# Optimization experiments

Measured on AMD Instinct MI355X. Metric: run time of the kernel, lower is better.

Reference implementation:

```python
import jax, jax.numpy as jnp
import numpy as np

B = 1024       # n_nodes
C = 128        # num_features (multiplicity of 0e in irreps_in)
L = 16         # num_ell = dim of coupling irreps 0e+1o+2e+3o
E = 10         # num_elements
Q = 3          # num_equivariance for 1o output (2*lmax+1)
# path counts (last dim of U tensors) per correlation order nu=1,2,3
P_0e = (1, 4, 23)
P_1o = (1, 6, 37)


def setup_inputs() -> dict:
    key = jax.random.key(0)
    ks = jax.random.split(key, 16)
    x = jax.random.normal(ks[0], (B, C, L), dtype=jnp.float32)
    elem = jax.random.randint(ks[1], (B,), 0, E)
    y = jax.nn.one_hot(elem, E, dtype=jnp.float32)  # one-hot element types
    # U tensors are constant (buffer) CG-derived coupling tensors; random stand-ins
    # with the exact shapes produced by U_matrix_real.
    U1_0e = jax.random.normal(ks[2], (L, P_0e[0]), dtype=jnp.float32)
    U2_0e = jax.random.normal(ks[3], (L, L, P_0e[1]), dtype=jnp.float32)
    U3_0e = jax.random.normal(ks[4], (L, L, L, P_0e[2]), dtype=jnp.float32)
    U1_1o = jax.random.normal(ks[5], (Q, L, P_1o[0]), dtype=jnp.float32)
    U2_1o = jax.random.normal(ks[6], (Q, L, L, P_1o[1]), dtype=jnp.float32)
    U3_1o = jax.random.normal(ks[7], (Q, L, L, L, P_1o[2]), dtype=jnp.float32)
    # per-element weights, init randn/num_params as in the torch module
    W1_0e = jax.random.normal(ks[8], (E, P_0e[0], C), dtype=jnp.float32) / P_0e[0]
    W2_0e = jax.random.normal(ks[9], (E, P_0e[1], C), dtype=jnp.float32) / P_0e[1]
    W3_0e = jax.random.normal(ks[10], (E, P_0e[2], C), dtype=jnp.float32) / P_0e[2]
    W1_1o = jax.random.normal(ks[11], (Q and E, P_1o[0], C), dtype=jnp.float32) / P_1o[0]
    W1_1o = jax.random.normal(ks[11], (E, P_1o[0], C), dtype=jnp.float32) / P_1o[0]
    W2_1o = jax.random.normal(ks[12], (E, P_1o[1], C), dtype=jnp.float32) / P_1o[1]
    W3_1o = jax.random.normal(ks[13], (E, P_1o[2], C), dtype=jnp.float32) / P_1o[2]
    return dict(x=x, y=y,
                U1_0e=U1_0e, U2_0e=U2_0e, U3_0e=U3_0e,
                W1_0e=W1_0e, W2_0e=W2_0e, W3_0e=W3_0e,
                U1_1o=U1_1o, U2_1o=U2_1o, U3_1o=U3_1o,
                W1_1o=W1_1o, W2_1o=W2_1o, W3_1o=W3_1o)


def _contract_0e(x, y, U1, U2, U3, W1, W2, W3):
    # correlation order 3 chain for a scalar (0e) output irrep
    out = jnp.einsum('wxik,ekc,bci,be->bcwx', U3, W3, x, y)            # [B,C,L,L]
    c = jnp.einsum('wxk,ekc,be->bcwx', U2, W2, y) + out
    out = jnp.einsum('bcwi,bci->bcw', c, x)                            # [B,C,L]
    c = jnp.einsum('wk,ekc,be->bcw', U1, W1, y) + out
    out = jnp.einsum('bci,bci->bc', c, x)                              # [B,C]
    return out


def _contract_1o(x, y, U1, U2, U3, W1, W2, W3):
    # correlation order 3 chain for a vector (1o) output irrep; w = equivariance dim (3)
    out = jnp.einsum('wxvik,ekc,bci,be->bcwxv', U3, W3, x, y)          # [B,C,3,L,L]
    c = jnp.einsum('wxvk,ekc,be->bcwxv', U2, W2, y) + out
    out = jnp.einsum('bcwxi,bci->bcwx', c, x)                          # [B,C,3,L]
    c = jnp.einsum('wxk,ekc,be->bcwx', U1, W1, y) + out
    out = jnp.einsum('bcwi,bci->bcw', c, x)                            # [B,C,3]
    return out.reshape(out.shape[0], -1)                                # [B,3C]


def reference(x, y, U1_0e, U2_0e, U3_0e, W1_0e, W2_0e, W3_0e,
              U1_1o, U2_1o, U3_1o, W1_1o, W2_1o, W3_1o):
    out0 = _contract_0e(x, y, U1_0e, U2_0e, U3_0e, W1_0e, W2_0e, W3_0e)
    out1 = _contract_1o(x, y, U1_1o, U2_1o, U3_1o, W1_1o, W2_1o, W3_1o)
    return jnp.concatenate([out0, out1], axis=-1)                       # [B, 4C]
```

## Files before the change

kernel.cpp:

```cpp
#include <hip/hip_runtime.h>

namespace {
constexpr int NB = 1024, NC = 128, NL = 16, NE = 10, NOUT = 4 * NC;
constexpr int NTHREADS = 256;
constexpr int NSPLIT = 2;
constexpr int P3_0 = 23, P2_0 = 4, P3_1 = 37, P2_1 = 6;
constexpr int TRI_P = 1040, DUO_P = 160, CSTRIDE = 1224;
constexpr int U3ROWS = P3_0 + 3 * P3_1;
constexpr int U2ROWS = P2_0 + 3 * P2_1;
constexpr int SYM3_FLOATS = U3ROWS * TRI_P;
constexpr int SYM2_FLOATS = U2ROWS * DUO_P;
constexpr int SYM_TOTAL = SYM3_FLOATS + SYM2_FLOATS;
constexpr int OFF_CNT = 0;
constexpr int OFF_NID = 16;
constexpr int OFF_SYM3A = 10272;
constexpr int OFF_SYM2A = OFF_SYM3A + SYM3_FLOATS;
constexpr int WS_REQ = OFF_SYM2A + SYM2_FLOATS;
}

__device__ __forceinline__ bool tri_from_padded(int t, int& ri, int& rj, int& rm) {
    int pos = 0;
    for (int i = 0; i < 16; ++i)
        for (int j = i; j < 16; ++j) {
            const int L = 16 - j, PL = (L + 3) & ~3;
            if (t < pos + PL) { ri = i; rj = j; rm = j + (t - pos); return (t - pos) < L; }
            pos += PL;
        }
    return false;
}
__device__ __forceinline__ bool duo_from_padded(int t, int& ri, int& rj) {
    int pos = 0;
    for (int i = 0; i < 16; ++i) {
        const int L = 16 - i, PL = (L + 3) & ~3;
        if (t < pos + PL) { ri = i; rj = i + (t - pos); return (t - pos) < L; }
        pos += PL;
    }
    return false;
}

__device__ __forceinline__ void sym_body(int n,
    const float* __restrict__ U3_0e, const float* __restrict__ U3_1o,
    const float* __restrict__ U2_0e, const float* __restrict__ U2_1o,
    float* __restrict__ dst) {
    if (n < SYM3_FLOATS) {
        const int kk = n / TRI_P, t = n - kk * TRI_P;
        int pass, k, P; const float* U;
        if (kk < P3_0) { pass = 0; k = kk; P = P3_0; U = U3_0e; }
        else { const int r = kk - P3_0; pass = 1 + r / P3_1; k = r - (pass - 1) * P3_1;
               P = P3_1; U = U3_1o + (size_t)(pass - 1) * 4096 * P3_1; }
        int i, j, m; float s = 0.f;
        if (tri_from_padded(t, i, j, m)) {
            auto u3 = [&](int a, int b, int c) {
                return U[(size_t)(((a << 4) + b) * 16 + c) * P + k]; };
            s = u3(i, j, m);
            if (i == j && j == m) {}
            else if (i == j) s += u3(i, m, i) + u3(m, i, i);
            else if (j == m) s += u3(j, i, j) + u3(j, j, i);
            else s += u3(i, m, j) + u3(j, i, m) + u3(j, m, i) + u3(m, i, j) + u3(m, j, i);
        }
        dst[n] = s;
    } else if (n < SYM_TOTAL) {
        const int r = n - SYM3_FLOATS;
        const int kk = r / DUO_P, t = r - kk * DUO_P;
        int pass, k, P; const float* U;
        if (kk < P2_0) { pass = 0; k = kk; P = P2_0; U = U2_0e; }
        else { const int q = kk - P2_0; pass = 1 + q / P2_1; k = q - (pass - 1) * P2_1;
               P = P2_1; U = U2_1o + (size_t)(pass - 1) * 256 * P2_1; }
        int i, j; float s = 0.f;
        if (duo_from_padded(t, i, j)) {
            auto u2 = [&](int a, int b) { return U[(size_t)((a << 4) + b) * P + k]; };
            s = u2(i, j) + (i < j ? u2(j, i) : 0.f);
        }
        dst[n] = s;
    }
}

__global__ void prep_kernel(const float* __restrict__ y,
                            const float* __restrict__ U3_0e, const float* __restrict__ U3_1o,
                            const float* __restrict__ U2_0e, const float* __restrict__ U2_1o,
                            float* __restrict__ ws) {
    const int bid = blockIdx.x, tid = threadIdx.x;
    if (bid < NE) {
        __shared__ int s_scan[NTHREADS];
        const int e = bid;
        unsigned pat = 0;
#pragma unroll
        for (int q = 0; q < 4; ++q)
            if (y[(tid * 4 + q) * NE + e] > 0.5f) pat |= (1u << q);
        const int lc = __popc(pat);
        s_scan[tid] = lc;
        __syncthreads();
#pragma unroll
        for (int off = 1; off < NTHREADS; off <<= 1) {
            const int add = (tid >= off) ? s_scan[tid - off] : 0;
            __syncthreads();
            s_scan[tid] += add;
            __syncthreads();
        }
        int* cnt = (int*)ws + OFF_CNT;
        int* nid = (int*)ws + OFF_NID + e * NB;
        int pos = s_scan[tid] - lc;
#pragma unroll
        for (int q = 0; q < 4; ++q)
            if (pat & (1u << q)) nid[pos++] = tid * 4 + q;
        if (tid == 0) cnt[e] = s_scan[NTHREADS - 1];
    } else {
        const int n = (bid - NE) * NTHREADS + tid;
        sym_body(n, U3_0e, U3_1o, U2_0e, U2_1o, ws + OFF_SYM3A);
    }
}

template <int P3c, int P2c>
__device__ __forceinline__ void build_lds(const float* __restrict__ sym3p,
                                          const float* __restrict__ sym2p,
                                          const float* __restrict__ s_w3,
                                          const float* __restrict__ s_w2,
                                          float* __restrict__ s_lds, int tid)
{
#pragma unroll 1
    for (int idx = tid; idx < (TRI_P / 4) * 2; idx += NTHREADS) {
        const int t4 = idx >> 1, cp = idx & 1;
        float aLx = 0, aLy = 0, aLz = 0, aLw = 0;
        float aHx = 0, aHy = 0, aHz = 0, aHw = 0;
#pragma unroll 4
        for (int k = 0; k < P3c; ++k) {
            const float4 u = *reinterpret_cast<const float4*>(sym3p + (size_t)k * TRI_P + 4 * t4);
            const float wL = s_w3[4 * k + 2 * cp];
            const float wH = s_w3[4 * k + 2 * cp + 1];
            aLx = fmaf(u.x, wL, aLx); aLy = fmaf(u.y, wL, aLy);
            aLz = fmaf(u.z, wL, aLz); aLw = fmaf(u.w, wL, aLw);
            aHx = fmaf(u.x, wH, aHx); aHy = fmaf(u.y, wH, aHy);
            aHz = fmaf(u.z, wH, aHz); aHw = fmaf(u.w, wH, aHw);
        }
        *reinterpret_cast<float4*>(s_lds + (2 * cp) * CSTRIDE + 4 * t4) =
            make_float4(aLx, aLy, aLz, aLw);
        *reinterpret_cast<float4*>(s_lds + (2 * cp + 1) * CSTRIDE + 4 * t4) =
            make_float4(aHx, aHy, aHz, aHw);
    }
    if (tid < (DUO_P / 4) * 2) {
        const int t4 = tid >> 1, cp = tid & 1;
        float aLx = 0, aLy = 0, aLz = 0, aLw = 0;
        float aHx = 0, aHy = 0, aHz = 0, aHw = 0;
#pragma unroll
        for (int k = 0; k < P2c; ++k) {
            const float4 u = *reinterpret_cast<const float4*>(sym2p + (size_t)k * DUO_P + 4 * t4);
            const float wL = s_w2[4 * k + 2 * cp];
            const float wH = s_w2[4 * k + 2 * cp + 1];
            aLx = fmaf(u.x, wL, aLx); aLy = fmaf(u.y, wL, aLy);
            aLz = fmaf(u.z, wL, aLz); aLw = fmaf(u.w, wL, aLw);
            aHx = fmaf(u.x, wH, aHx); aHy = fmaf(u.y, wH, aHy);
            aHz = fmaf(u.z, wH, aHz); aHw = fmaf(u.w, wH, aHw);
        }
        *reinterpret_cast<float4*>(s_lds + (2 * cp) * CSTRIDE + TRI_P + 4 * t4) =
            make_float4(aLx, aLy, aLz, aLw);
        *reinterpret_cast<float4*>(s_lds + (2 * cp + 1) * CSTRIDE + TRI_P + 4 * t4) =
            make_float4(aHx, aHy, aHz, aHw);
    }
}

__global__ void __launch_bounds__(NTHREADS, 4) node_kernel(
    const float* __restrict__ x, const float* __restrict__ ws,
    const float* __restrict__ U1_0e, const float* __restrict__ U1_1o,
    const float* __restrict__ W1_0e, const float* __restrict__ W2_0e,
    const float* __restrict__ W3_0e,
    const float* __restrict__ W1_1o, const float* __restrict__ W2_1o,
    const float* __restrict__ W3_1o,
    float* __restrict__ out) {
    __shared__ __align__(16) float s_lds[4 * CSTRIDE];
    __shared__ __align__(16) float s_w3[4 * P3_1];
    __shared__ __align__(16) float s_w2[4 * P2_1];
    __shared__ int s_nid[NB];
    const int tid = threadIdx.x, bid = blockIdx.x;
    const int pass = bid / (NE * (NC / 4));
    const int rest = bid % (NE * (NC / 4));
    const int e = rest / (NC / 4);
    const int cg = (rest % (NC / 4)) * 4;

    const int P3c = pass == 0 ? P3_0 : P3_1;
    const int P2c = pass == 0 ? P2_0 : P2_1;
    const int k3b = pass == 0 ? 0 : P3_0 + (pass - 1) * P3_1;
    const int k2b = pass == 0 ? 0 : P2_0 + (pass - 1) * P2_1;
    const float* W3e = (pass == 0 ? W3_0e + (size_t)e * P3_0 * NC
                                  : W3_1o + (size_t)e * P3_1 * NC) + cg;
    const float* W2e = (pass == 0 ? W2_0e + (size_t)e * P2_0 * NC
                                  : W2_1o + (size_t)e * P2_1 * NC) + cg;
    const float* W1e = (pass == 0 ? W1_0e : W1_1o) + e * NC + cg;
    const float* U1p = pass == 0 ? U1_0e : U1_1o + (pass - 1) * NL;
    const float* sym3p = ws + OFF_SYM3A + (size_t)k3b * TRI_P;
    const float* sym2p = ws + OFF_SYM2A + (size_t)k2b * DUO_P;

    const int* cnt = (const int*)ws + OFF_CNT;
    const int* nid = (const int*)ws + OFF_NID + e * NB;
    const int nn = cnt[e];
    for (int i = tid; i < nn; i += NTHREADS) s_nid[i] = nid[i];

    if (tid < P3c) {
        *reinterpret_cast<float4*>(&s_w3[4 * tid]) =
            *reinterpret_cast<const float4*>(W3e + tid * NC);
    } else if (tid >= 64 && tid < 64 + P2c) {
        const int k = tid - 64;
        *reinterpret_cast<float4*>(&s_w2[4 * k]) =
            *reinterpret_cast<const float4*>(W2e + k * NC);
    } else if (tid >= 128 && tid < 192) {
        const int t = tid - 128;
        s_lds[(t >> 4) * CSTRIDE + 1200 + (t & 15)] = U1p[t & 15] * W1e[t >> 4];
    }
    __syncthreads();

    if (pass == 0) build_lds<P3_0, P2_0>(sym3p, sym2p, s_w3, s_w2, s_lds, tid);
    else           build_lds<P3_1, P2_1>(sym3p, sym2p, s_w3, s_w2, s_lds, tid);
    __syncthreads();

    const int w = tid >> 6;
    const int lane = tid & 63;
    const int cc = cg + w;
    const float* Tch = s_lds + w * CSTRIDE;
    const int col = pass == 0 ? cc : NC + 3 * cc + (pass - 1);

#pragma unroll 1
    for (int base = 0; base < nn; base += 64) {
        const int slot = base + lane;
        const bool val = slot < nn;
        const int b = s_nid[val ? slot : 0];
        const float* xp = x + ((size_t)b * NC + cc) * NL;
        float xr[NL];
#pragma unroll
        for (int v4 = 0; v4 < 4; ++v4)
            reinterpret_cast<float4*>(xr)[v4] = reinterpret_cast<const float4*>(xp)[v4];

        float acc = 0.f;
        int t3 = 0, t2 = 0;
#pragma unroll
        for (int i = 0; i < 16; ++i) {
            float gi = Tch[1200 + i];
            const int L2 = 16 - i, PL2 = (L2 + 3) & ~3;
            float s2r[16];
#pragma unroll
            for (int q4 = 0; q4 < PL2 / 4; ++q4)
                reinterpret_cast<float4*>(s2r)[q4] =
                    *reinterpret_cast<const float4*>(Tch + TRI_P + t2 + 4 * q4);
            t2 += PL2;
#pragma unroll
            for (int jo = 0; jo < 16 - i; ++jo) {
                const int j = i + jo;
                float wv = s2r[jo];
                const int Lr = 16 - j, PLr = (Lr + 3) & ~3;
#pragma unroll
                for (int q4 = 0; q4 < PLr / 4; ++q4) {
                    const float4 tv = *reinterpret_cast<const float4*>(Tch + t3 + 4 * q4);
                    wv = fmaf(tv.x, xr[(j + 4 * q4 + 0) & 15], wv);
                    wv = fmaf(tv.y, xr[(j + 4 * q4 + 1) & 15], wv);
                    wv = fmaf(tv.z, xr[(j + 4 * q4 + 2) & 15], wv);
                    wv = fmaf(tv.w, xr[(j + 4 * q4 + 3) & 15], wv);
                }
                t3 += PLr;
                gi = fmaf(wv, xr[j], gi);
            }
            acc = fmaf(gi, xr[i], acc);
        }
        if (val) out[(size_t)b * NOUT + col] = acc;
    }
}

template <int P3, int P2>
__device__ __forceinline__ void build_gather_f(const float* __restrict__ U3,
                                               const float* __restrict__ U2,
                                               const float* __restrict__ s_w3,
                                               const float* __restrict__ s_w2,
                                               float* __restrict__ lds, int tid) {
#pragma unroll 1
    for (int t = tid; t < TRI_P; t += NTHREADS) {
        int i, j, m; const bool v = tri_from_padded(t, i, j, m);
        float a0 = 0, a1 = 0, a2 = 0, a3 = 0;
        if (v) {
            int ng = 1, g1 = 0, g2 = 0, g3 = 0, g4 = 0, g5 = 0;
            const int g0 = ((i * 16 + j) * 16 + m);
            if (i == j && j == m) { ng = 1; }
            else if (i == j) { g1 = ((i * 16 + m) * 16 + i); g2 = ((m * 16 + i) * 16 + i); ng = 3; }
            else if (j == m) { g1 = ((j * 16 + i) * 16 + j); g2 = ((j * 16 + j) * 16 + i); ng = 3; }
            else { g1 = ((i * 16 + m) * 16 + j); g2 = ((j * 16 + i) * 16 + m);
                   g3 = ((j * 16 + m) * 16 + i); g4 = ((m * 16 + i) * 16 + j);
                   g5 = ((m * 16 + j) * 16 + i); ng = 6; }
#pragma unroll 1
            for (int k = 0; k < P3; ++k) {
                float u = U3[(size_t)g0 * P3 + k];
                if (ng > 1) u += U3[(size_t)g1 * P3 + k] + U3[(size_t)g2 * P3 + k];
                if (ng == 6) u += U3[(size_t)g3 * P3 + k] + U3[(size_t)g4 * P3 + k]
                                + U3[(size_t)g5 * P3 + k];
                const float4 wk = reinterpret_cast<const float4*>(s_w3)[k];
                a0 = fmaf(u, wk.x, a0); a1 = fmaf(u, wk.y, a1);
                a2 = fmaf(u, wk.z, a2); a3 = fmaf(u, wk.w, a3);
            }
        }
        lds[0 * CSTRIDE + t] = a0; lds[1 * CSTRIDE + t] = a1;
        lds[2 * CSTRIDE + t] = a2; lds[3 * CSTRIDE + t] = a3;
    }
    if (tid < DUO_P) {
        int i, j; const bool v = duo_from_padded(tid, i, j);
        float a0 = 0, a1 = 0, a2 = 0, a3 = 0;
        if (v) {
#pragma unroll 1
            for (int k = 0; k < P2; ++k) {
                float u = U2[(size_t)((i << 4) + j) * P2 + k];
                if (i < j) u += U2[(size_t)((j << 4) + i) * P2 + k];
                const float4 wk = reinterpret_cast<const float4*>(s_w2)[k];
                a0 = fmaf(u, wk.x, a0); a1 = fmaf(u, wk.y, a1);
                a2 = fmaf(u, wk.z, a2); a3 = fmaf(u, wk.w, a3);
            }
        }
        lds[0 * CSTRIDE + TRI_P + tid] = a0; lds[1 * CSTRIDE + TRI_P + tid] = a1;
        lds[2 * CSTRIDE + TRI_P + tid] = a2; lds[3 * CSTRIDE + TRI_P + tid] = a3;
    }
}

__global__ void __launch_bounds__(NTHREADS, 4) symcon_fallback(
    const float* __restrict__ x, const float* __restrict__ y,
    const float* __restrict__ U1_0e, const float* __restrict__ U2_0e,
    const float* __restrict__ U3_0e,
    const float* __restrict__ W1_0e, const float* __restrict__ W2_0e,
    const float* __restrict__ W3_0e,
    const float* __restrict__ U1_1o, const float* __restrict__ U2_1o,
    const float* __restrict__ U3_1o,
    const float* __restrict__ W1_1o, const float* __restrict__ W2_1o,
    const float* __restrict__ W3_1o,
    float* __restrict__ out)
{
    __shared__ __align__(16) float s_lds[4 * CSTRIDE];
    __shared__ __align__(16) float s_w3[4 * P3_1 + 4];
    __shared__ __align__(16) float s_w2[4 * P2_1];
    __shared__ int s_nid[NB];
    __shared__ int s_scan[NTHREADS];

    const int tid = threadIdx.x;
    const int bid = blockIdx.x;
    const int s   = bid & 1;
    const int e   = (bid >> 1) % NE;
    const int cg  = (bid / (2 * NE)) * 4;

    unsigned pat = 0;
#pragma unroll
    for (int q = 0; q < 4; ++q)
        if (y[(tid * 4 + q) * NE + e] > 0.5f) pat |= (1u << q);
    const int lc = __popc(pat);
    s_scan[tid] = lc;
    __syncthreads();
#pragma unroll
    for (int off = 1; off < NTHREADS; off <<= 1) {
        const int add = (tid >= off) ? s_scan[tid - off] : 0;
        __syncthreads();
        s_scan[tid] += add;
        __syncthreads();
    }
    const int nn = s_scan[NTHREADS - 1];
    {
        int pos = s_scan[tid] - lc;
#pragma unroll
        for (int q = 0; q < 4; ++q)
            if (pat & (1u << q)) s_nid[pos++] = tid * 4 + q;
    }
    __syncthreads();

    const int half = (nn + 1) >> 1;
    const int l0 = s * half, l1 = min(nn, l0 + half);
    const int L = l1 - l0;
    if (L <= 0) return;

    const int w    = tid >> 6;
    const int ch   = (tid >> 4) & 3;
    const int nsub = tid & 15;
    const int cc   = cg + ch;
    const int chunk = (L + 3) >> 2;
    const int wbase = l0 + w * chunk;
    const int wend  = min(l1, wbase + chunk);
    const int iters = (chunk + 15) >> 4;
    const float* Tch = s_lds + ch * CSTRIDE;

#pragma unroll 1
    for (int pass = 0; pass < 4; ++pass) {
        const float* U3r = pass == 0 ? U3_0e : U3_1o + (size_t)(pass - 1) * 4096 * P3_1;
        const float* U2r = pass == 0 ? U2_0e : U2_1o + (size_t)(pass - 1) * 256 * P2_1;
        const float* U1p = (pass == 0 ? U1_0e : U1_1o + (pass - 1) * NL);
        const float* W3e = (pass == 0 ? W3_0e + (size_t)e * P3_0 * NC
                                      : W3_1o + (size_t)e * P3_1 * NC) + cg;
        const float* W2e = (pass == 0 ? W2_0e + (size_t)e * P2_0 * NC
                                      : W2_1o + (size_t)e * P2_1 * NC) + cg;
        const float* W1e = (pass == 0 ? W1_0e : W1_1o) + e * NC + cg;
        const int P3c = pass == 0 ? P3_0 : P3_1;
        const int P2c = pass == 0 ? P2_0 : P2_1;
        const int col = pass == 0 ? cc : NC + 3 * cc + (pass - 1);

        if (tid < 4 * P3c) {
            s_w3[tid] = W3e[(tid >> 2) * NC + (tid & 3)];
        } else if (tid >= 152 && tid < 152 + 4 * P2c) {
            const int t = tid - 152;
            s_w2[t] = W2e[(t >> 2) * NC + (t & 3)];
        } else if (tid >= 192) {
            const int t = tid - 192;
            s_lds[(t >> 4) * CSTRIDE + 1200 + (t & 15)] = U1p[t & 15] * W1e[t >> 4];
        }
        __syncthreads();

        if (pass == 0) build_gather_f<P3_0, P2_0>(U3r, U2r, s_w3, s_w2, s_lds, tid);
        else           build_gather_f<P3_1, P2_1>(U3r, U2r, s_w3, s_w2, s_lds, tid);
        __syncthreads();

#pragma unroll 1
        for (int it = 0; it < iters; ++it) {
            const int slot = wbase + it * 16 + nsub;
            const bool val = slot < wend;
            const int b = s_nid[val ? slot : l0];
            const float* xp = x + ((size_t)b * NC + cc) * NL;
            float xr[NL];
#pragma unroll
            for (int v4 = 0; v4 < 4; ++v4)
                reinterpret_cast<float4*>(xr)[v4] = reinterpret_cast<const float4*>(xp)[v4];

            float acc = 0.f;
            int t3 = 0, t2 = 0;
#pragma unroll
            for (int i = 0; i < 16; ++i) {
                float gi = Tch[1200 + i];
                const int L2 = 16 - i, PL2 = (L2 + 3) & ~3;
                float s2r[16];
#pragma unroll
                for (int q4 = 0; q4 < PL2 / 4; ++q4)
                    reinterpret_cast<float4*>(s2r)[q4] =
                        *reinterpret_cast<const float4*>(Tch + TRI_P + t2 + 4 * q4);
                t2 += PL2;
#pragma unroll
                for (int jo = 0; jo < 16 - i; ++jo) {
                    const int j = i + jo;
                    float wv = s2r[jo];
                    const int Lr = 16 - j, PLr = (Lr + 3) & ~3;
#pragma unroll
                    for (int q4 = 0; q4 < PLr / 4; ++q4) {
                        const float4 tv = *reinterpret_cast<const float4*>(Tch + t3 + 4 * q4);
                        wv = fmaf(tv.x, xr[(j + 4 * q4 + 0) & 15], wv);
                        wv = fmaf(tv.y, xr[(j + 4 * q4 + 1) & 15], wv);
                        wv = fmaf(tv.z, xr[(j + 4 * q4 + 2) & 15], wv);
                        wv = fmaf(tv.w, xr[(j + 4 * q4 + 3) & 15], wv);
                    }
                    t3 += PLr;
                    gi = fmaf(wv, xr[j], gi);
                }
                acc = fmaf(gi, xr[i], acc);
            }
            if (val) out[(size_t)b * NOUT + col] = acc;
        }
        __syncthreads();
    }
}

extern "C" void kernel_launch(void* const* d_in, const int* in_sizes, int n_in,
                              void* d_out, int out_size, void* d_ws, size_t ws_size,
                              hipStream_t stream) {
    const float* x     = (const float*)d_in[0];
    const float* y     = (const float*)d_in[1];
    const float* U1_0e = (const float*)d_in[2];
    const float* U2_0e = (const float*)d_in[3];
    const float* U3_0e = (const float*)d_in[4];
    const float* W1_0e = (const float*)d_in[5];
    const float* W2_0e = (const float*)d_in[6];
    const float* W3_0e = (const float*)d_in[7];
    const float* U1_1o = (const float*)d_in[8];
    const float* U2_1o = (const float*)d_in[9];
    const float* U3_1o = (const float*)d_in[10];
    const float* W1_1o = (const float*)d_in[11];
    const float* W2_1o = (const float*)d_in[12];
    const float* W3_1o = (const float*)d_in[13];
    float* out = (float*)d_out;
    float* ws = (float*)d_ws;

    if (ws_size >= (size_t)WS_REQ * sizeof(float)) {
        const int symBlocks = (SYM_TOTAL + NTHREADS - 1) / NTHREADS;
        hipLaunchKernelGGL(prep_kernel, dim3(NE + symBlocks), dim3(NTHREADS), 0, stream,
                           y, U3_0e, U3_1o, U2_0e, U2_1o, ws);
        hipLaunchKernelGGL(node_kernel, dim3(4 * NE * (NC / 4)), dim3(NTHREADS), 0, stream,
                           x, ws, U1_0e, U1_1o, W1_0e, W2_0e, W3_0e,
                           W1_1o, W2_1o, W3_1o, out);
    } else {
        hipLaunchKernelGGL(symcon_fallback, dim3(NE * (NC / 4) * NSPLIT), dim3(NTHREADS), 0, stream,
                           x, y, U1_0e, U2_0e, U3_0e, W1_0e, W2_0e, W3_0e,
                           U1_1o, U2_1o, U3_1o, W1_1o, W2_1o, W3_1o, out);
    }
}
```

Before: 89.31 us.

## Store contracted order-3 coupling tensor in LDS as packed bf16

```diff
diff --git a/kernel.cpp b/kernel.cpp
--- a/kernel.cpp
+++ b/kernel.cpp
@@ -6,9 +6,14 @@
 constexpr int NSPLIT = 2;
 constexpr int P3_0 = 23, P2_0 = 4, P3_1 = 37, P2_1 = 6;
 constexpr int TRI_P = 1040, DUO_P = 160, CSTRIDE = 1224;
+constexpr int TRI_P8 = 1376;
+constexpr int TRI_W = TRI_P8 / 2;
+constexpr int S2_OFF = TRI_W;
+constexpr int S1_OFF = S2_OFF + DUO_P;
+constexpr int CSTRIDE_U = 872;
 constexpr int U3ROWS = P3_0 + 3 * P3_1;
 constexpr int U2ROWS = P2_0 + 3 * P2_1;
-constexpr int SYM3_FLOATS = U3ROWS * TRI_P;
+constexpr int SYM3_FLOATS = U3ROWS * TRI_P8;
 constexpr int SYM2_FLOATS = U2ROWS * DUO_P;
 constexpr int SYM_TOTAL = SYM3_FLOATS + SYM2_FLOATS;
 constexpr int OFF_CNT = 0;
@@ -18,6 +23,28 @@
 constexpr int WS_REQ = OFF_SYM2A + SYM2_FLOATS;
 }
 
+__device__ __forceinline__ unsigned bfpack(float a, float b) {
+    unsigned ua = __float_as_uint(a); ua = (ua + 0x7FFFu + ((ua >> 16) & 1u)) >> 16;
+    unsigned ub = __float_as_uint(b); ub = (ub + 0x7FFFu + ((ub >> 16) & 1u)) >> 16;
+    return ua | (ub << 16);
+}
+__device__ __forceinline__ void bfun8(uint4 p, float* __restrict__ f) {
+    f[0] = __uint_as_float(p.x << 16); f[1] = __uint_as_float(p.x & 0xffff0000u);
+    f[2] = __uint_as_float(p.y << 16); f[3] = __uint_as_float(p.y & 0xffff0000u);
+    f[4] = __uint_as_float(p.z << 16); f[5] = __uint_as_float(p.z & 0xffff0000u);
+    f[6] = __uint_as_float(p.w << 16); f[7] = __uint_as_float(p.w & 0xffff0000u);
+}
+
+__device__ __forceinline__ bool tri_from_padded8(int t, int& ri, int& rj, int& rm) {
+    int pos = 0;
+    for (int i = 0; i < 16; ++i)
+        for (int j = i; j < 16; ++j) {
+            const int L = 16 - j, PL = (L + 7) & ~7;
+            if (t < pos + PL) { ri = i; rj = j; rm = j + (t - pos); return (t - pos) < L; }
+            pos += PL;
+        }
+    return false;
+}
 __device__ __forceinline__ bool tri_from_padded(int t, int& ri, int& rj, int& rm) {
     int pos = 0;
     for (int i = 0; i < 16; ++i)
@@ -43,13 +70,13 @@
     const float* __restrict__ U2_0e, const float* __restrict__ U2_1o,
     float* __restrict__ dst) {
     if (n < SYM3_FLOATS) {
-        const int kk = n / TRI_P, t = n - kk * TRI_P;
+        const int kk = n / TRI_P8, t = n - kk * TRI_P8;
         int pass, k, P; const float* U;
         if (kk < P3_0) { pass = 0; k = kk; P = P3_0; U = U3_0e; }
         else { const int r = kk - P3_0; pass = 1 + r / P3_1; k = r - (pass - 1) * P3_1;
                P = P3_1; U = U3_1o + (size_t)(pass - 1) * 4096 * P3_1; }
         int i, j, m; float s = 0.f;
-        if (tri_from_padded(t, i, j, m)) {
+        if (tri_from_padded8(t, i, j, m)) {
             auto u3 = [&](int a, int b, int c) {
                 return U[(size_t)(((a << 4) + b) * 16 + c) * P + k]; };
             s = u3(i, j, m);
@@ -115,16 +142,17 @@
                                           const float* __restrict__ sym2p,
                                           const float* __restrict__ s_w3,
                                           const float* __restrict__ s_w2,
-                                          float* __restrict__ s_lds, int tid)
+                                          unsigned* __restrict__ s_ldsu, int tid)
 {
-#pragma unroll 1
-    for (int idx = tid; idx < (TRI_P / 4) * 2; idx += NTHREADS) {
+    float* s_ldsf = reinterpret_cast<float*>(s_ldsu);
+#pragma unroll 1
+    for (int idx = tid; idx < (TRI_P8 / 4) * 2; idx += NTHREADS) {
         const int t4 = idx >> 1, cp = idx & 1;
         float aLx = 0, aLy = 0, aLz = 0, aLw = 0;
         float aHx = 0, aHy = 0, aHz = 0, aHw = 0;
 #pragma unroll 4
         for (int k = 0; k < P3c; ++k) {
-            const float4 u = *reinterpret_cast<const float4*>(sym3p + (size_t)k * TRI_P + 4 * t4);
+            const float4 u = *reinterpret_cast<const float4*>(sym3p + (size_t)k * TRI_P8 + 4 * t4);
             const float wL = s_w3[4 * k + 2 * cp];
             const float wH = s_w3[4 * k + 2 * cp + 1];
             aLx = fmaf(u.x, wL, aLx); aLy = fmaf(u.y, wL, aLy);
@@ -132,10 +160,10 @@
             aHx = fmaf(u.x, wH, aHx); aHy = fmaf(u.y, wH, aHy);
             aHz = fmaf(u.z, wH, aHz); aHw = fmaf(u.w, wH, aHw);
         }
-        *reinterpret_cast<float4*>(s_lds + (2 * cp) * CSTRIDE + 4 * t4) =
-            make_float4(aLx, aLy, aLz, aLw);
-        *reinterpret_cast<float4*>(s_lds + (2 * cp + 1) * CSTRIDE + 4 * t4) =
-            make_float4(aHx, aHy, aHz, aHw);
+        *reinterpret_cast<uint2*>(s_ldsu + (2 * cp) * CSTRIDE_U + 2 * t4) =
+            make_uint2(bfpack(aLx, aLy), bfpack(aLz, aLw));
+        *reinterpret_cast<uint2*>(s_ldsu + (2 * cp + 1) * CSTRIDE_U + 2 * t4) =
+            make_uint2(bfpack(aHx, aHy), bfpack(aHz, aHw));
     }
     if (tid < (DUO_P / 4) * 2) {
         const int t4 = tid >> 1, cp = tid & 1;
@@ -151,9 +179,9 @@
             aHx = fmaf(u.x, wH, aHx); aHy = fmaf(u.y, wH, aHy);
             aHz = fmaf(u.z, wH, aHz); aHw = fmaf(u.w, wH, aHw);
         }
-        *reinterpret_cast<float4*>(s_lds + (2 * cp) * CSTRIDE + TRI_P + 4 * t4) =
+        *reinterpret_cast<float4*>(s_ldsf + (2 * cp) * CSTRIDE_U + S2_OFF + 4 * t4) =
             make_float4(aLx, aLy, aLz, aLw);
-        *reinterpret_cast<float4*>(s_lds + (2 * cp + 1) * CSTRIDE + TRI_P + 4 * t4) =
+        *reinterpret_cast<float4*>(s_ldsf + (2 * cp + 1) * CSTRIDE_U + S2_OFF + 4 * t4) =
             make_float4(aHx, aHy, aHz, aHw);
     }
 }
@@ -166,10 +194,11 @@
     const float* __restrict__ W1_1o, const float* __restrict__ W2_1o,
     const float* __restrict__ W3_1o,
     float* __restrict__ out) {
-    __shared__ __align__(16) float s_lds[4 * CSTRIDE];
+    __shared__ __align__(16) unsigned s_ldsu[4 * CSTRIDE_U];
     __shared__ __align__(16) float s_w3[4 * P3_1];
     __shared__ __align__(16) float s_w2[4 * P2_1];
     __shared__ int s_nid[NB];
+    float* s_ldsf = reinterpret_cast<float*>(s_ldsu);
     const int tid = threadIdx.x, bid = blockIdx.x;
     const int pass = bid / (NE * (NC / 4));
     const int rest = bid % (NE * (NC / 4));
@@ -186,7 +215,7 @@
                                   : W2_1o + (size_t)e * P2_1 * NC) + cg;
     const float* W1e = (pass == 0 ? W1_0e : W1_1o) + e * NC + cg;
     const float* U1p = pass == 0 ? U1_0e : U1_1o + (pass - 1) * NL;
-    const float* sym3p = ws + OFF_SYM3A + (size_t)k3b * TRI_P;
+    const float* sym3p = ws + OFF_SYM3A + (size_t)k3b * TRI_P8;
     const float* sym2p = ws + OFF_SYM2A + (size_t)k2b * DUO_P;
 
     const int* cnt = (const int*)ws + OFF_CNT;
@@ -203,18 +232,19 @@
             *reinterpret_cast<const float4*>(W2e + k * NC);
     } else if (tid >= 128 && tid < 192) {
         const int t = tid - 128;
-        s_lds[(t >> 4) * CSTRIDE + 1200 + (t & 15)] = U1p[t & 15] * W1e[t >> 4];
+        s_ldsf[(t >> 4) * CSTRIDE_U + S1_OFF + (t & 15)] = U1p[t & 15] * W1e[t >> 4];
     }
     __syncthreads();
 
-    if (pass == 0) build_lds<P3_0, P2_0>(sym3p, sym2p, s_w3, s_w2, s_lds, tid);
-    else           build_lds<P3_1, P2_1>(sym3p, sym2p, s_w3, s_w2, s_lds, tid);
+    if (pass == 0) build_lds<P3_0, P2_0>(sym3p, sym2p, s_w3, s_w2, s_ldsu, tid);
+    else           build_lds<P3_1, P2_1>(sym3p, sym2p, s_w3, s_w2, s_ldsu, tid);
     __syncthreads();
 
     const int w = tid >> 6;
     const int lane = tid & 63;
     const int cc = cg + w;
-    const float* Tch = s_lds + w * CSTRIDE;
+    const unsigned* Tchu = s_ldsu + w * CSTRIDE_U;
+    const float* Tchf = reinterpret_cast<const float*>(Tchu);
     const int col = pass == 0 ? cc : NC + 3 * cc + (pass - 1);
 
 #pragma unroll 1
@@ -232,28 +262,37 @@
         int t3 = 0, t2 = 0;
 #pragma unroll
         for (int i = 0; i < 16; ++i) {
-            float gi = Tch[1200 + i];
+            float gi = Tchf[S1_OFF + i];
             const int L2 = 16 - i, PL2 = (L2 + 3) & ~3;
             float s2r[16];
 #pragma unroll
             for (int q4 = 0; q4 < PL2 / 4; ++q4)
                 reinterpret_cast<float4*>(s2r)[q4] =
-                    *reinterpret_cast<const float4*>(Tch + TRI_P + t2 + 4 * q4);
+                    *reinterpret_cast<const float4*>(Tchf + S2_OFF + t2 + 4 * q4);
             t2 += PL2;
 #pragma unroll
             for (int jo = 0; jo < 16 - i; ++jo) {
                 const int j = i + jo;
                 float wv = s2r[jo];
-                const int Lr = 16 - j, PLr = (Lr + 3) & ~3;
-#pragma unroll
-                for (int q4 = 0; q4 < PLr / 4; ++q4) {
-                    const float4 tv = *reinterpret_cast<const float4*>(Tch + t3 + 4 * q4);
-                    wv = fmaf(tv.x, xr[(j + 4 * q4 + 0) & 15], wv);
-                    wv = fmaf(tv.y, xr[(j + 4 * q4 + 1) & 15], wv);
-                    wv = fmaf(tv.z, xr[(j + 4 * q4 + 2) & 15], wv);
-                    wv = fmaf(tv.w, xr[(j + 4 * q4 + 3) & 15], wv);
+                {
+                    const uint4 p0 = *reinterpret_cast<const uint4*>(Tchu + t3);
+                    float f[8];
+                    bfun8(p0, f);
+#pragma unroll
+                    for (int m8 = 0; m8 < 8; ++m8)
+                        wv = fmaf(f[m8], xr[(j + m8) & 15], wv);
                 }
-                t3 += PLr;
+                if (j < 8) {
+                    const uint4 p1 = *reinterpret_cast<const uint4*>(Tchu + t3 + 4);
+                    float f[8];
+                    bfun8(p1, f);
+#pragma unroll
+                    for (int m8 = 0; m8 < 8; ++m8)
+                        wv = fmaf(f[m8], xr[(j + 8 + m8) & 15], wv);
+                    t3 += 8;
+                } else {
+                    t3 += 4;
+                }
                 gi = fmaf(wv, xr[j], gi);
             }
             acc = fmaf(gi, xr[i], acc);
```

New measurement: 239.1 us. +167.7%, slower.
